# Kernel tuning notes

Hardware: AMD Instinct MI355X
Metric: run time of the kernel (lower is better)

The kernel has to match this reference:

```python
import jax, jax.numpy as jnp
import numpy as np

B, L, D, H = 2, 256, 512, 8
DH = D // H
EPS = 1e-12
NEG = -1000000000000000.0


def setup_inputs() -> dict:
    key = jax.random.key(0)
    ks = jax.random.split(key, 16)
    s = 0.02
    return {
        "inputs": jax.random.normal(ks[0], (B, L, D), jnp.float32),
        "pos_embedding": jax.random.normal(ks[1], (B, L, L, D), jnp.float32),
        "seq_mask": jnp.ones((B, L), jnp.int32),
        "Wq": jax.random.normal(ks[2], (D, D), jnp.float32) * s,
        "bq": jnp.zeros((D,), jnp.float32),
        "Wk": jax.random.normal(ks[3], (D, D), jnp.float32) * s,
        "bk": jnp.zeros((D,), jnp.float32),
        "Wv": jax.random.normal(ks[4], (D, D), jnp.float32) * s,
        "bv": jnp.zeros((D,), jnp.float32),
        "Wr": jax.random.normal(ks[5], (D, D), jnp.float32) * s,
        "br": jnp.zeros((D,), jnp.float32),
        "u": jax.random.normal(ks[6], (H, DH), jnp.float32),
        "v": jax.random.normal(ks[7], (H, DH), jnp.float32),
        "Wf": jax.random.normal(ks[8], (D, D), jnp.float32) * s,
        "bf": jnp.zeros((D,), jnp.float32),
        "gamma": jnp.ones((D,), jnp.float32),
        "beta": jnp.zeros((D,), jnp.float32),
    }


def _layer_norm(x, gamma, beta, eps):
    mu = jnp.mean(x, axis=-1, keepdims=True)
    var = jnp.mean(jnp.square(x - mu), axis=-1, keepdims=True)
    return (x - mu) * jax.lax.rsqrt(var + eps) * gamma + beta


def reference(inputs, pos_embedding, seq_mask, Wq, bq, Wk, bk, Wv, bv, Wr, br,
              u, v, Wf, bf, gamma, beta):
    b, l, d = inputs.shape
    # projections (nn.Linear: x @ W.T + b)
    q = (inputs @ Wq.T + bq).reshape(b, l, H, DH).transpose(0, 2, 1, 3)  # [B,H,L,DH]
    k = (inputs @ Wk.T + bk).reshape(b, l, H, DH).transpose(0, 2, 1, 3)
    vv = (inputs @ Wv.T + bv).reshape(b, l, H, DH).transpose(0, 2, 1, 3)
    rel = (pos_embedding @ Wr.T + br).reshape(b, l, l, H, DH)            # [B,L,L,H,DH]

    # A + C: content-content + content-bias
    A_C = jnp.einsum('bhid,bhjd->bhij', q + u[None, :, None, :], k)
    # B + D: position term against per-(i,j) relative embeddings
    B_D = jnp.einsum('bhid,bijhd->bhij', q + v[None, :, None, :], rel)

    score = (A_C + B_D) / np.sqrt(DH).astype(np.float32)
    invalid = (seq_mask == 0)[:, None, None, :]   # mask keys where seq_mask==0
    score = jnp.where(invalid, NEG, score)
    attn = jax.nn.softmax(score, axis=-1)

    ctx = jnp.einsum('bhij,bhjd->bhid', attn, vv)
    ctx = ctx.transpose(0, 2, 1, 3).reshape(b, l, d)

    # FFN (single dense) + residual + LayerNorm
    h = ctx @ Wf.T + bf
    return _layer_norm(h + inputs, gamma, beta, EPS)
```

## Files before the change

### kernel.cpp

```cpp
#include <hip/hip_runtime.h>
#include <cmath>

typedef __bf16 bf16x8 __attribute__((ext_vector_type(8)));
typedef float f32x4 __attribute__((ext_vector_type(4)));

__device__ __forceinline__ float4 ld4(const float* p) { return *reinterpret_cast<const float4*>(p); }
__device__ __forceinline__ void st4(float* p, float4 v) { *reinterpret_cast<float4*>(p) = v; }
__device__ __forceinline__ void fma4(float4& a, float s, const float4& v) {
    a.x = fmaf(s, v.x, a.x); a.y = fmaf(s, v.y, a.y);
    a.z = fmaf(s, v.z, a.z); a.w = fmaf(s, v.w, a.w);
}
__device__ __forceinline__ float dot4(const float4& a, const float4& b) {
    return a.x*b.x + a.y*b.y + a.z*b.z + a.w*b.w;
}
__device__ __forceinline__ unsigned short f2bf(float f) {
    unsigned int x = __float_as_uint(f);
    unsigned int r = x + 0x7FFFu + ((x >> 16) & 1u);
    return (unsigned short)(r >> 16);
}
__device__ __forceinline__ ushort4 cvt4u(float4 a) {
    ushort4 u;
    u.x = f2bf(a.x); u.y = f2bf(a.y); u.z = f2bf(a.z); u.w = f2bf(a.w);
    return u;
}
__device__ __forceinline__ bf16x8 cvt8(float4 a, float4 b) {
    bf16x8 r;
    r[0] = (__bf16)a.x; r[1] = (__bf16)a.y; r[2] = (__bf16)a.z; r[3] = (__bf16)a.w;
    r[4] = (__bf16)b.x; r[5] = (__bf16)b.y; r[6] = (__bf16)b.z; r[7] = (__bf16)b.w;
    return r;
}

__device__ __forceinline__ void mfma_tile(
        const float* __restrict__ Abase, int ldA,
        const float* __restrict__ Bbase, int ldB,
        int K, int lane, f32x4 acc[4]) {
    int koff = (lane >> 4) * 8;
    int rr = lane & 15;
    const float* ap = Abase + rr * ldA + koff;
    const float* bp = Bbase + rr * ldB + koff;
#pragma unroll 2
    for (int k0 = 0; k0 < K; k0 += 32) {
        float4 a0  = ld4(ap + k0),            a1  = ld4(ap + k0 + 4);
        float4 b00 = ld4(bp + k0),            b01 = ld4(bp + k0 + 4);
        float4 b10 = ld4(bp + 16*ldB + k0),   b11 = ld4(bp + 16*ldB + k0 + 4);
        float4 b20 = ld4(bp + 32*ldB + k0),   b21 = ld4(bp + 32*ldB + k0 + 4);
        float4 b30 = ld4(bp + 48*ldB + k0),   b31 = ld4(bp + 48*ldB + k0 + 4);
        bf16x8 af = cvt8(a0, a1);
        acc[0] = __builtin_amdgcn_mfma_f32_16x16x32_bf16(af, cvt8(b00, b01), acc[0], 0, 0, 0);
        acc[1] = __builtin_amdgcn_mfma_f32_16x16x32_bf16(af, cvt8(b10, b11), acc[1], 0, 0, 0);
        acc[2] = __builtin_amdgcn_mfma_f32_16x16x32_bf16(af, cvt8(b20, b21), acc[2], 0, 0, 0);
        acc[3] = __builtin_amdgcn_mfma_f32_16x16x32_bf16(af, cvt8(b30, b31), acc[3], 0, 0, 0);
    }
}

__global__ __launch_bounds__(256) void k_front(
        const float* __restrict__ x,
        const float* __restrict__ Wq, const float* __restrict__ Wk, const float* __restrict__ Wv,
        const float* __restrict__ bq, const float* __restrict__ bk, const float* __restrict__ bv,
        const float* __restrict__ Wr,
        float* __restrict__ qw, float* __restrict__ kw, float* __restrict__ vw,
        float* __restrict__ wrt) {
    int id = blockIdx.x;
    int t = threadIdx.x;
    if (id < 192) {
        int mat = id >> 6, rem = id & 63;
        int m0 = (rem >> 3) * 64, n0 = (rem & 7) * 64;
        const float* W   = (mat == 0) ? Wq : (mat == 1) ? Wk : Wv;
        const float* bias= (mat == 0) ? bq : (mat == 1) ? bk : bv;
        float* out       = (mat == 0) ? qw : (mat == 1) ? kw : vw;
        int wv = t >> 6, lane = t & 63;
        f32x4 acc[4] = {{0,0,0,0},{0,0,0,0},{0,0,0,0},{0,0,0,0}};
        mfma_tile(x + (m0 + wv * 16) * 512, 512, W + n0 * 512, 512, 512, lane, acc);
        int h = n0 >> 6;
        int col = lane & 15, rbase = (lane >> 4) * 4;
#pragma unroll
        for (int c = 0; c < 4; c++) {
            int d = c * 16 + col;
            float bv_ = bias[n0 + d];
#pragma unroll
            for (int r = 0; r < 4; r++) {
                int m = m0 + wv * 16 + rbase + r;
                int b = m >> 8, i = m & 255;
                out[((b * 8 + h) * 256 + i) * 64 + d] = acc[c][r] + bv_;
            }
        }
    } else {
        __shared__ float tile[64][65];
        int id2 = id - 192;
        int n0 = (id2 >> 3) * 64, k0 = (id2 & 7) * 64;
        int tx = t & 63, ty = t >> 6;
#pragma unroll
        for (int r = 0; r < 16; r++) {
            int row = ty * 16 + r;
            tile[row][tx] = Wr[(n0 + row) * 512 + k0 + tx];
        }
        __syncthreads();
#pragma unroll
        for (int r = 0; r < 16; r++) {
            int row = ty * 16 + r;
            wrt[(k0 + row) * 512 + n0 + tx] = tile[tx][row];
        }
    }
}

__global__ __launch_bounds__(256) void k_mid(
        const float* __restrict__ qw, const float* __restrict__ kw,
        const float* __restrict__ wrt,
        const float* __restrict__ u, const float* __restrict__ vb, const float* __restrict__ br,
        float* __restrict__ w_ws, float* __restrict__ ac_ws) {
    int id = blockIdx.x;
    int t = threadIdx.x, wv = t >> 6, lane = t & 63;
    __shared__ float red[8][64];
    if (id < 512) {
        int h = id >> 6, rem = id & 63;
        int m0 = (rem >> 3) * 64, n0 = (rem & 7) * 64;
        int b = m0 >> 8, i0 = m0 & 255;
        {
            int e = t & 63, grp = t >> 6;
            const float* wr_row = wrt + (size_t)(n0 + e) * 512 + h * 64 + grp * 16;
            const float* vbh = vb + h * 64 + grp * 16;
            float s = 0.f;
#pragma unroll
            for (int d = 0; d < 16; d += 4) s += dot4(ld4(wr_row + d), ld4(vbh + d));
            red[grp][e] = s;
        }
        __syncthreads();
        __shared__ float vwr_l[64];
        if (t < 64) vwr_l[t] = red[0][t] + red[1][t] + red[2][t] + red[3][t];
        f32x4 acc[4] = {{0,0,0,0},{0,0,0,0},{0,0,0,0},{0,0,0,0}};
        mfma_tile(qw + ((b * 8 + h) * 256 + i0 + wv * 16) * 64, 64,
                  wrt + (size_t)n0 * 512 + h * 64, 512, 64, lane, acc);
        __syncthreads();
        int col = lane & 15, rbase = (lane >> 4) * 4;
#pragma unroll
        for (int c = 0; c < 4; c++) {
            float vw_ = vwr_l[c * 16 + col];
            int n = n0 + c * 16 + col;
#pragma unroll
            for (int r = 0; r < 4; r++) {
                int m = m0 + wv * 16 + rbase + r;
                w_ws[((size_t)m * 8 + h) * 512 + n] = acc[c][r] + vw_;
            }
        }
    } else {
        int id2 = id - 512;
        int bh = id2 >> 4, rem2 = id2 & 15;
        int b = bh >> 3, h = bh & 7;
        int i0 = (rem2 >> 2) * 64, j0 = (rem2 & 3) * 64;
        {
            int xx = t & 63, grp = t >> 6;
            const float* qrow = qw + ((b * 8 + h) * 256 + i0 + xx) * 64 + grp * 16;
            const float* brh = br + h * 64 + grp * 16;
            const float* vbh = vb + h * 64 + grp * 16;
            float s = 0.f;
#pragma unroll
            for (int d = 0; d < 16; d += 4) {
                float4 q4 = ld4(qrow + d), b4 = ld4(brh + d), v4 = ld4(vbh + d);
                s += (q4.x + v4.x) * b4.x + (q4.y + v4.y) * b4.y
                   + (q4.z + v4.z) * b4.z + (q4.w + v4.w) * b4.w;
            }
            red[grp][xx] = s;
            const float* krow = kw + ((b * 8 + h) * 256 + j0 + xx) * 64 + grp * 16;
            const float* uh = u + h * 64 + grp * 16;
            s = 0.f;
#pragma unroll
            for (int d = 0; d < 16; d += 4) s += dot4(ld4(krow + d), ld4(uh + d));
            red[4 + grp][xx] = s;
        }
        __syncthreads();
        __shared__ float c_l[64], uk_l[64];
        if (t < 64) c_l[t] = red[0][t] + red[1][t] + red[2][t] + red[3][t];
        else if (t < 128) { int y = t - 64; uk_l[y] = red[4][y] + red[5][y] + red[6][y] + red[7][y]; }
        f32x4 acc[4] = {{0,0,0,0},{0,0,0,0},{0,0,0,0},{0,0,0,0}};
        mfma_tile(qw + ((b * 8 + h) * 256 + i0 + wv * 16) * 64, 64,
                  kw + ((b * 8 + h) * 256 + j0) * 64, 64, 64, lane, acc);
        __syncthreads();
        int col = lane & 15, rbase = (lane >> 4) * 4;
#pragma unroll
        for (int c = 0; c < 4; c++) {
            int j = j0 + c * 16 + col;
            float ukv = uk_l[c * 16 + col];
#pragma unroll
            for (int r = 0; r < 4; r++) {
                int ii = wv * 16 + rbase + r;
                ac_ws[((b * 256 + i0 + ii) * 8 + h) * 256 + j] = acc[c][r] + ukv + c_l[ii];
            }
        }
    }
}

__global__ __launch_bounds__(512, 4) void k_attn(
        const float* __restrict__ pos, const float* __restrict__ w_ws,
        const float* __restrict__ ac_ws, const float* __restrict__ vw,
        const int* __restrict__ seq_mask, float* __restrict__ ctx) {
    int bi = blockIdx.x;
    int b = bi >> 8, i = bi & 255;
    int t = threadIdx.x;
    int wv = t >> 6, lane = t & 63;
    __shared__ unsigned short wl[8 * 512];
    __shared__ float sc[8][256];
    __shared__ unsigned short stage[8][4096];

    {
        int h = t >> 6;
        int e0 = (t & 63) * 8;
        const float* src = w_ws + ((size_t)bi * 8 + h) * 512 + e0;
        float4 a = ld4(src);
        float4 c = ld4(src + 4);
        *reinterpret_cast<ushort4*>(&wl[h * 512 + e0])     = cvt4u(a);
        *reinterpret_cast<ushort4*>(&wl[h * 512 + e0 + 4]) = cvt4u(c);
    }
    __syncthreads();

    const float* pb = pos + (size_t)bi * (256 * 512);
    int jbase = wv * 32;
    unsigned short* sb = &stage[wv][0];
    int arow = lane & 15;
    int koff = (lane >> 4) * 8;

#pragma unroll
    for (int jt = 0; jt < 2; jt++) {
        f32x4 acc = {0, 0, 0, 0};
#pragma unroll
        for (int eh = 0; eh < 2; eh++) {
            const float* src = pb + (size_t)(jbase + jt * 16) * 512 + eh * 256 + lane * 4;
            float4 tmp[16];
#pragma unroll
            for (int s = 0; s < 16; s++) tmp[s] = ld4(src + s * 512);
#pragma unroll
            for (int s = 0; s < 16; s++) {
                *reinterpret_cast<ushort4*>(&sb[s * 256 + lane * 4]) = cvt4u(tmp[s]);
            }
#pragma unroll
            for (int es = 0; es < 8; es++) {
                bf16x8 af = *reinterpret_cast<const bf16x8*>(&sb[arow * 256 + es * 32 + koff]);
                bf16x8 bf = *reinterpret_cast<const bf16x8*>(&wl[(lane & 7) * 512 + (eh * 8 + es) * 32 + koff]);
                acc = __builtin_amdgcn_mfma_f32_16x16x32_bf16(af, bf, acc, 0, 0, 0);
            }
        }
        int h = lane & 15;
        int rbase = (lane >> 4) * 4;
        if (h < 8) {
#pragma unroll
            for (int r = 0; r < 4; r++) sc[h][jbase + jt * 16 + rbase + r] = acc[r];
        }
    }
    __syncthreads();

    {
        int h = wv;
        const float* acrow = ac_ws + ((b * 256 + i) * 8 + h) * 256;
        float vals[4];
        float mx = -INFINITY;
#pragma unroll
        for (int r = 0; r < 4; r++) {
            int j = lane + r * 64;
            float s = (sc[h][j] + acrow[j]) * 0.125f;
            if (seq_mask[b * 256 + j] == 0) s = -1e15f;
            vals[r] = s;
            mx = fmaxf(mx, s);
        }
#pragma unroll
        for (int m = 32; m >= 1; m >>= 1) mx = fmaxf(mx, __shfl_xor(mx, m, 64));
        float sum = 0.f;
#pragma unroll
        for (int r = 0; r < 4; r++) { vals[r] = __expf(vals[r] - mx); sum += vals[r]; }
#pragma unroll
        for (int m = 32; m >= 1; m >>= 1) sum += __shfl_xor(sum, m, 64);
        float inv = 1.0f / sum;
#pragma unroll
        for (int r = 0; r < 4; r++) sc[h][lane + r * 64] = vals[r] * inv;
    }

    float4* part = reinterpret_cast<float4*>(&stage[0][0]);
    {
        int h = wv;
        int d4 = (lane & 15) * 4;
        int js = lane >> 4;
        const float* vbase = vw + (size_t)(b * 8 + h) * 256 * 64 + d4;
        float4 acc = {0, 0, 0, 0};
#pragma unroll 2
        for (int r = 0; r < 64; r += 4) {
            int j = js * 64 + r;
            float p0 = sc[h][j + 0], p1 = sc[h][j + 1];
            float p2 = sc[h][j + 2], p3 = sc[h][j + 3];
            float4 v0 = ld4(vbase + (size_t)(j + 0) * 64);
            float4 v1 = ld4(vbase + (size_t)(j + 1) * 64);
            float4 v2 = ld4(vbase + (size_t)(j + 2) * 64);
            float4 v3 = ld4(vbase + (size_t)(j + 3) * 64);
            fma4(acc, p0, v0); fma4(acc, p1, v1);
            fma4(acc, p2, v2); fma4(acc, p3, v3);
        }
        part[(h * 4 + js) * 16 + (lane & 15)] = acc;
    }
    {
        int h = wv;
        if ((lane >> 4) == 0) {
            int l = lane & 15;
            float4 a0 = part[(h * 4 + 0) * 16 + l], a1 = part[(h * 4 + 1) * 16 + l];
            float4 a2 = part[(h * 4 + 2) * 16 + l], a3 = part[(h * 4 + 3) * 16 + l];
            float4 o;
            o.x = a0.x + a1.x + a2.x + a3.x;
            o.y = a0.y + a1.y + a2.y + a3.y;
            o.z = a0.z + a1.z + a2.z + a3.z;
            o.w = a0.w + a1.w + a2.w + a3.w;
            st4(ctx + (size_t)(b * 256 + i) * 512 + h * 64 + l * 4, o);
        }
    }
}

__global__ __launch_bounds__(256) void k_ffn(
        const float* __restrict__ A, const float* __restrict__ Wf,
        const float* __restrict__ bias, const float* __restrict__ resid,
        float* __restrict__ outp) {
    int m0 = blockIdx.x * 64, n0 = blockIdx.y * 64;
    int t = threadIdx.x, wv = t >> 6, lane = t & 63;
    f32x4 acc[4] = {{0,0,0,0},{0,0,0,0},{0,0,0,0},{0,0,0,0}};
    mfma_tile(A + (m0 + wv * 16) * 512, 512, Wf + n0 * 512, 512, 512, lane, acc);
    int col = lane & 15, rbase = (lane >> 4) * 4;
#pragma unroll
    for (int c = 0; c < 4; c++) {
        int n = n0 + c * 16 + col;
        float bv_ = bias[n];
#pragma unroll
        for (int r = 0; r < 4; r++) {
            int m = m0 + wv * 16 + rbase + r;
            outp[m * 512 + n] = acc[c][r] + bv_ + resid[m * 512 + n];
        }
    }
}

__global__ __launch_bounds__(256) void k_ln(
        const float* __restrict__ tmp, const float* __restrict__ gamma,
        const float* __restrict__ beta, float* __restrict__ out) {
    int m = blockIdx.x, t = threadIdx.x;
    int wv = t >> 6, lane = t & 63;
    float2 xv = *reinterpret_cast<const float2*>(&tmp[m * 512 + t * 2]);
    __shared__ float red[4];
    float s = xv.x + xv.y;
#pragma unroll
    for (int k = 32; k >= 1; k >>= 1) s += __shfl_xor(s, k, 64);
    if (lane == 0) red[wv] = s;
    __syncthreads();
    float mu = (red[0] + red[1] + red[2] + red[3]) * (1.0f / 512.0f);
    __syncthreads();
    float dx = xv.x - mu, dy = xv.y - mu;
    float vs = dx * dx + dy * dy;
#pragma unroll
    for (int k = 32; k >= 1; k >>= 1) vs += __shfl_xor(vs, k, 64);
    if (lane == 0) red[wv] = vs;
    __syncthreads();
    float var = (red[0] + red[1] + red[2] + red[3]) * (1.0f / 512.0f);
    float rstd = rsqrtf(var + 1e-12f);
    float2 g = *reinterpret_cast<const float2*>(&gamma[t * 2]);
    float2 be = *reinterpret_cast<const float2*>(&beta[t * 2]);
    float2 o;
    o.x = dx * rstd * g.x + be.x;
    o.y = dy * rstd * g.y + be.y;
    *reinterpret_cast<float2*>(&out[m * 512 + t * 2]) = o;
}

extern "C" void kernel_launch(void* const* d_in, const int* in_sizes, int n_in,
                              void* d_out, int out_size, void* d_ws, size_t ws_size,
                              hipStream_t stream) {
    const float* x     = (const float*)d_in[0];
    const float* pos   = (const float*)d_in[1];
    const int*   smask = (const int*)d_in[2];
    const float* Wq = (const float*)d_in[3];
    const float* bq = (const float*)d_in[4];
    const float* Wk = (const float*)d_in[5];
    const float* bk = (const float*)d_in[6];
    const float* Wv = (const float*)d_in[7];
    const float* bv = (const float*)d_in[8];
    const float* Wr = (const float*)d_in[9];
    const float* br = (const float*)d_in[10];
    const float* u  = (const float*)d_in[11];
    const float* vb = (const float*)d_in[12];
    const float* Wf = (const float*)d_in[13];
    const float* bf = (const float*)d_in[14];
    const float* gamma = (const float*)d_in[15];
    const float* beta  = (const float*)d_in[16];
    float* out = (float*)d_out;

    float* ws = (float*)d_ws;
    float* q_ws   = ws;
    float* k_ws   = q_ws  + 262144;
    float* v_ws   = k_ws  + 262144;
    float* w_ws   = v_ws  + 262144;
    float* ac_ws  = w_ws  + 2097152;
    float* ctx_ws = ac_ws + 1048576;
    float* tmp_ws = ctx_ws + 262144;
    float* wrt_ws = tmp_ws + 262144;

    k_front<<<dim3(256), 256, 0, stream>>>(x, Wq, Wk, Wv, bq, bk, bv, Wr,
                                           q_ws, k_ws, v_ws, wrt_ws);
    k_mid<<<dim3(768), 256, 0, stream>>>(q_ws, k_ws, wrt_ws, u, vb, br, w_ws, ac_ws);
    k_attn<<<dim3(512), 512, 0, stream>>>(pos, w_ws, ac_ws, v_ws, smask, ctx_ws);
    k_ffn<<<dim3(8, 8), 256, 0, stream>>>(ctx_ws, Wf, bf, x, tmp_ws);
    k_ln<<<dim3(512), 256, 0, stream>>>(tmp_ws, gamma, beta, out);
}
```

Measured before the change: 110.7 us.

## Fuse FFN with LayerNorm, drop Wr transpose, swizzle attention LDS staging

Removes the separate Wr transpose pass: k_mid reads Wr directly with strided scalar loads, and the (q+v)·br bias term moves into the Q projection epilogue. The u·k and v·Wr terms are folded into the MFMA A operand by adding the bias vectors before conversion. In k_attn the staging buffer is halved, an XOR swizzle is applied to LDS addresses to reduce bank conflicts, and the occupancy hint goes from 4 to 6. The FFN and LayerNorm kernels are fused into one 32-block kernel that computes LN statistics with a single-pass sum/sumsq. Risks are low parallelism in the fused output kernel, uncoalesced Wr reads, and sumsq variance cancellation.

```diff
diff --git a/kernel.cpp b/kernel.cpp
--- a/kernel.cpp
+++ b/kernel.cpp
@@ -5,14 +5,12 @@
 typedef float f32x4 __attribute__((ext_vector_type(4)));
 
 __device__ __forceinline__ float4 ld4(const float* p) { return *reinterpret_cast<const float4*>(p); }
+__device__ __forceinline__ float2 ld2(const float* p) { return *reinterpret_cast<const float2*>(p); }
 __device__ __forceinline__ void st4(float* p, float4 v) { *reinterpret_cast<float4*>(p) = v; }
 __device__ __forceinline__ void fma4(float4& a, float s, const float4& v) {
     a.x = fmaf(s, v.x, a.x); a.y = fmaf(s, v.y, a.y);
     a.z = fmaf(s, v.z, a.z); a.w = fmaf(s, v.w, a.w);
 }
-__device__ __forceinline__ float dot4(const float4& a, const float4& b) {
-    return a.x*b.x + a.y*b.y + a.z*b.z + a.w*b.w;
-}
 __device__ __forceinline__ unsigned short f2bf(float f) {
     unsigned int x = __float_as_uint(f);
     unsigned int r = x + 0x7FFFu + ((x >> 16) & 1u);
@@ -22,6 +20,9 @@
     ushort4 u;
     u.x = f2bf(a.x); u.y = f2bf(a.y); u.z = f2bf(a.z); u.w = f2bf(a.w);
     return u;
+}
+__device__ __forceinline__ ushort2 cvt2u(float2 a) {
+    ushort2 u; u.x = f2bf(a.x); u.y = f2bf(a.y); return u;
 }
 __device__ __forceinline__ bf16x8 cvt8(float4 a, float4 b) {
     bf16x8 r;
@@ -57,139 +58,139 @@
         const float* __restrict__ x,
         const float* __restrict__ Wq, const float* __restrict__ Wk, const float* __restrict__ Wv,
         const float* __restrict__ bq, const float* __restrict__ bk, const float* __restrict__ bv,
-        const float* __restrict__ Wr,
+        const float* __restrict__ vbv, const float* __restrict__ br,
         float* __restrict__ qw, float* __restrict__ kw, float* __restrict__ vw,
-        float* __restrict__ wrt) {
+        float* __restrict__ c_ws) {
     int id = blockIdx.x;
     int t = threadIdx.x;
-    if (id < 192) {
-        int mat = id >> 6, rem = id & 63;
-        int m0 = (rem >> 3) * 64, n0 = (rem & 7) * 64;
-        const float* W   = (mat == 0) ? Wq : (mat == 1) ? Wk : Wv;
-        const float* bias= (mat == 0) ? bq : (mat == 1) ? bk : bv;
-        float* out       = (mat == 0) ? qw : (mat == 1) ? kw : vw;
-        int wv = t >> 6, lane = t & 63;
-        f32x4 acc[4] = {{0,0,0,0},{0,0,0,0},{0,0,0,0},{0,0,0,0}};
-        mfma_tile(x + (m0 + wv * 16) * 512, 512, W + n0 * 512, 512, 512, lane, acc);
-        int h = n0 >> 6;
-        int col = lane & 15, rbase = (lane >> 4) * 4;
-#pragma unroll
-        for (int c = 0; c < 4; c++) {
-            int d = c * 16 + col;
-            float bv_ = bias[n0 + d];
+    int mat = id >> 6, rem = id & 63;
+    int m0 = (rem >> 3) * 64, n0 = (rem & 7) * 64;
+    const float* W   = (mat == 0) ? Wq : (mat == 1) ? Wk : Wv;
+    const float* bias= (mat == 0) ? bq : (mat == 1) ? bk : bv;
+    float* out       = (mat == 0) ? qw : (mat == 1) ? kw : vw;
+    int wv = t >> 6, lane = t & 63;
+    f32x4 acc[4] = {{0,0,0,0},{0,0,0,0},{0,0,0,0},{0,0,0,0}};
+    mfma_tile(x + (m0 + wv * 16) * 512, 512, W + n0 * 512, 512, 512, lane, acc);
+    int h = n0 >> 6;
+    int col = lane & 15, rbase = (lane >> 4) * 4;
+    float cpart[4] = {0, 0, 0, 0};
+#pragma unroll
+    for (int c = 0; c < 4; c++) {
+        int d = c * 16 + col;
+        float bv_ = bias[n0 + d];
+        float vbd = vbv[n0 + d];
+        float brd = br[n0 + d];
+#pragma unroll
+        for (int r = 0; r < 4; r++) {
+            int m = m0 + wv * 16 + rbase + r;
+            int b = m >> 8, i = m & 255;
+            float q = acc[c][r] + bv_;
+            out[((b * 8 + h) * 256 + i) * 64 + d] = q;
+            cpart[r] += (q + vbd) * brd;
+        }
+    }
+    if (mat == 0) {
+#pragma unroll
+        for (int msk = 1; msk < 16; msk <<= 1) {
+#pragma unroll
+            for (int r = 0; r < 4; r++) cpart[r] += __shfl_xor(cpart[r], msk, 64);
+        }
+        if (col == 0) {
 #pragma unroll
             for (int r = 0; r < 4; r++) {
                 int m = m0 + wv * 16 + rbase + r;
                 int b = m >> 8, i = m & 255;
-                out[((b * 8 + h) * 256 + i) * 64 + d] = acc[c][r] + bv_;
-            }
-        }
-    } else {
-        __shared__ float tile[64][65];
-        int id2 = id - 192;
-        int n0 = (id2 >> 3) * 64, k0 = (id2 & 7) * 64;
-        int tx = t & 63, ty = t >> 6;
-#pragma unroll
-        for (int r = 0; r < 16; r++) {
-            int row = ty * 16 + r;
-            tile[row][tx] = Wr[(n0 + row) * 512 + k0 + tx];
-        }
-        __syncthreads();
-#pragma unroll
-        for (int r = 0; r < 16; r++) {
-            int row = ty * 16 + r;
-            wrt[(k0 + row) * 512 + n0 + tx] = tile[tx][row];
+                c_ws[(b * 8 + h) * 256 + i] = cpart[r];
+            }
         }
     }
 }
 
 __global__ __launch_bounds__(256) void k_mid(
         const float* __restrict__ qw, const float* __restrict__ kw,
-        const float* __restrict__ wrt,
-        const float* __restrict__ u, const float* __restrict__ vb, const float* __restrict__ br,
+        const float* __restrict__ Wr,
+        const float* __restrict__ u, const float* __restrict__ vbv,
+        const float* __restrict__ c_ws,
         float* __restrict__ w_ws, float* __restrict__ ac_ws) {
     int id = blockIdx.x;
     int t = threadIdx.x, wv = t >> 6, lane = t & 63;
-    __shared__ float red[8][64];
-    if (id < 512) {
-        int h = id >> 6, rem = id & 63;
-        int m0 = (rem >> 3) * 64, n0 = (rem & 7) * 64;
+    int rr = lane & 15, koff = (lane >> 4) * 8;
+    int col = lane & 15, rbase = (lane >> 4) * 4;
+    if (id < 256) {
+        int h = id >> 5, rem = id & 31;
+        int it = rem >> 2, et2 = rem & 3;
+        int m0 = it * 64, E0 = et2 * 128;
         int b = m0 >> 8, i0 = m0 & 255;
-        {
-            int e = t & 63, grp = t >> 6;
-            const float* wr_row = wrt + (size_t)(n0 + e) * 512 + h * 64 + grp * 16;
-            const float* vbh = vb + h * 64 + grp * 16;
-            float s = 0.f;
-#pragma unroll
-            for (int d = 0; d < 16; d += 4) s += dot4(ld4(wr_row + d), ld4(vbh + d));
-            red[grp][e] = s;
-        }
-        __syncthreads();
-        __shared__ float vwr_l[64];
-        if (t < 64) vwr_l[t] = red[0][t] + red[1][t] + red[2][t] + red[3][t];
-        f32x4 acc[4] = {{0,0,0,0},{0,0,0,0},{0,0,0,0},{0,0,0,0}};
-        mfma_tile(qw + ((b * 8 + h) * 256 + i0 + wv * 16) * 64, 64,
-                  wrt + (size_t)n0 * 512 + h * 64, 512, 64, lane, acc);
-        __syncthreads();
-        int col = lane & 15, rbase = (lane >> 4) * 4;
-#pragma unroll
-        for (int c = 0; c < 4; c++) {
-            float vw_ = vwr_l[c * 16 + col];
-            int n = n0 + c * 16 + col;
+        const float* ap = qw + (size_t)((b * 8 + h) * 256 + i0 + wv * 16 + rr) * 64;
+        const float* vb_p = vbv + h * 64;
+        f32x4 acc[8];
+#pragma unroll
+        for (int nt = 0; nt < 8; nt++) acc[nt] = (f32x4){0, 0, 0, 0};
+#pragma unroll
+        for (int k0 = 0; k0 < 64; k0 += 32) {
+            float4 a0 = ld4(ap + k0 + koff), a1 = ld4(ap + k0 + koff + 4);
+            float4 v0 = ld4(vb_p + k0 + koff), v1 = ld4(vb_p + k0 + koff + 4);
+            a0.x += v0.x; a0.y += v0.y; a0.z += v0.z; a0.w += v0.w;
+            a1.x += v1.x; a1.y += v1.y; a1.z += v1.z; a1.w += v1.w;
+            bf16x8 af = cvt8(a0, a1);
+            const float* wrb = Wr + (size_t)(h * 64 + k0 + koff) * 512 + E0 + rr;
+#pragma unroll
+            for (int nt = 0; nt < 8; nt++) {
+                bf16x8 bf_;
+#pragma unroll
+                for (int kk = 0; kk < 8; kk++)
+                    bf_[kk] = (__bf16)wrb[(size_t)kk * 512 + nt * 16];
+                acc[nt] = __builtin_amdgcn_mfma_f32_16x16x32_bf16(af, bf_, acc[nt], 0, 0, 0);
+            }
+        }
+#pragma unroll
+        for (int nt = 0; nt < 8; nt++) {
+            int e = E0 + nt * 16 + col;
 #pragma unroll
             for (int r = 0; r < 4; r++) {
                 int m = m0 + wv * 16 + rbase + r;
-                w_ws[((size_t)m * 8 + h) * 512 + n] = acc[c][r] + vw_;
+                w_ws[((size_t)m * 8 + h) * 512 + e] = acc[nt][r];
             }
         }
     } else {
-        int id2 = id - 512;
-        int bh = id2 >> 4, rem2 = id2 & 15;
+        int id2 = id - 256;
+        int bh = id2 >> 3, rem = id2 & 7;
         int b = bh >> 3, h = bh & 7;
-        int i0 = (rem2 >> 2) * 64, j0 = (rem2 & 3) * 64;
-        {
-            int xx = t & 63, grp = t >> 6;
-            const float* qrow = qw + ((b * 8 + h) * 256 + i0 + xx) * 64 + grp * 16;
-            const float* brh = br + h * 64 + grp * 16;
-            const float* vbh = vb + h * 64 + grp * 16;
-            float s = 0.f;
-#pragma unroll
-            for (int d = 0; d < 16; d += 4) {
-                float4 q4 = ld4(qrow + d), b4 = ld4(brh + d), v4 = ld4(vbh + d);
-                s += (q4.x + v4.x) * b4.x + (q4.y + v4.y) * b4.y
-                   + (q4.z + v4.z) * b4.z + (q4.w + v4.w) * b4.w;
-            }
-            red[grp][xx] = s;
-            const float* krow = kw + ((b * 8 + h) * 256 + j0 + xx) * 64 + grp * 16;
-            const float* uh = u + h * 64 + grp * 16;
-            s = 0.f;
-#pragma unroll
-            for (int d = 0; d < 16; d += 4) s += dot4(ld4(krow + d), ld4(uh + d));
-            red[4 + grp][xx] = s;
-        }
-        __syncthreads();
-        __shared__ float c_l[64], uk_l[64];
-        if (t < 64) c_l[t] = red[0][t] + red[1][t] + red[2][t] + red[3][t];
-        else if (t < 128) { int y = t - 64; uk_l[y] = red[4][y] + red[5][y] + red[6][y] + red[7][y]; }
-        f32x4 acc[4] = {{0,0,0,0},{0,0,0,0},{0,0,0,0},{0,0,0,0}};
-        mfma_tile(qw + ((b * 8 + h) * 256 + i0 + wv * 16) * 64, 64,
-                  kw + ((b * 8 + h) * 256 + j0) * 64, 64, 64, lane, acc);
-        __syncthreads();
-        int col = lane & 15, rbase = (lane >> 4) * 4;
-#pragma unroll
-        for (int c = 0; c < 4; c++) {
-            int j = j0 + c * 16 + col;
-            float ukv = uk_l[c * 16 + col];
-#pragma unroll
-            for (int r = 0; r < 4; r++) {
-                int ii = wv * 16 + rbase + r;
-                ac_ws[((b * 256 + i0 + ii) * 8 + h) * 256 + j] = acc[c][r] + ukv + c_l[ii];
-            }
-        }
-    }
-}
-
-__global__ __launch_bounds__(512, 4) void k_attn(
+        int i0 = (rem >> 1) * 64, J0 = (rem & 1) * 128;
+        const float* ap = qw + (size_t)((b * 8 + h) * 256 + i0 + wv * 16 + rr) * 64;
+        const float* up = u + h * 64;
+        const float* kbase = kw + (size_t)((b * 8 + h) * 256 + J0) * 64;
+        f32x4 acc[8];
+#pragma unroll
+        for (int nt = 0; nt < 8; nt++) acc[nt] = (f32x4){0, 0, 0, 0};
+#pragma unroll
+        for (int k0 = 0; k0 < 64; k0 += 32) {
+            float4 a0 = ld4(ap + k0 + koff), a1 = ld4(ap + k0 + koff + 4);
+            float4 u0 = ld4(up + k0 + koff), u1 = ld4(up + k0 + koff + 4);
+            a0.x += u0.x; a0.y += u0.y; a0.z += u0.z; a0.w += u0.w;
+            a1.x += u1.x; a1.y += u1.y; a1.z += u1.z; a1.w += u1.w;
+            bf16x8 af = cvt8(a0, a1);
+#pragma unroll
+            for (int nt = 0; nt < 8; nt++) {
+                const float* kp = kbase + (size_t)(nt * 16 + rr) * 64 + k0 + koff;
+                bf16x8 bf_ = cvt8(ld4(kp), ld4(kp + 4));
+                acc[nt] = __builtin_amdgcn_mfma_f32_16x16x32_bf16(af, bf_, acc[nt], 0, 0, 0);
+            }
+        }
+#pragma unroll
+        for (int r = 0; r < 4; r++) {
+            int i = i0 + wv * 16 + rbase + r;
+            float ci = c_ws[(b * 8 + h) * 256 + i];
+#pragma unroll
+            for (int nt = 0; nt < 8; nt++) {
+                int j = J0 + nt * 16 + col;
+                ac_ws[((size_t)(b * 256 + i) * 8 + h) * 256 + j] = acc[nt][r] + ci;
+            }
+        }
+    }
+}
+
+__global__ __launch_bounds__(512, 6) void k_attn(
         const float* __restrict__ pos, const float* __restrict__ w_ws,
         const float* __restrict__ ac_ws, const float* __restrict__ vw,
         const int* __restrict__ seq_mask, float* __restrict__ ctx) {
@@ -199,22 +200,22 @@
     int wv = t >> 6, lane = t & 63;
     __shared__ unsigned short wl[8 * 512];
     __shared__ float sc[8][256];
-    __shared__ unsigned short stage[8][4096];
+    __shared__ unsigned short stage[8][2048];
 
     {
         int h = t >> 6;
         int e0 = (t & 63) * 8;
         const float* src = w_ws + ((size_t)bi * 8 + h) * 512 + e0;
-        float4 a = ld4(src);
-        float4 c = ld4(src + 4);
-        *reinterpret_cast<ushort4*>(&wl[h * 512 + e0])     = cvt4u(a);
-        *reinterpret_cast<ushort4*>(&wl[h * 512 + e0 + 4]) = cvt4u(c);
+        float4 a = ld4(src), c = ld4(src + 4);
+        int byte = ((h * 512 + e0) * 2) ^ ((h & 7) << 4);
+        *reinterpret_cast<ushort4*>(reinterpret_cast<char*>(wl) + byte)     = cvt4u(a);
+        *reinterpret_cast<ushort4*>(reinterpret_cast<char*>(wl) + byte + 8) = cvt4u(c);
     }
     __syncthreads();
 
     const float* pb = pos + (size_t)bi * (256 * 512);
     int jbase = wv * 32;
-    unsigned short* sb = &stage[wv][0];
+    char* sb = reinterpret_cast<char*>(&stage[wv][0]);
     int arow = lane & 15;
     int koff = (lane >> 4) * 8;
 
@@ -222,20 +223,25 @@
     for (int jt = 0; jt < 2; jt++) {
         f32x4 acc = {0, 0, 0, 0};
 #pragma unroll
-        for (int eh = 0; eh < 2; eh++) {
-            const float* src = pb + (size_t)(jbase + jt * 16) * 512 + eh * 256 + lane * 4;
-            float4 tmp[16];
-#pragma unroll
-            for (int s = 0; s < 16; s++) tmp[s] = ld4(src + s * 512);
+        for (int eh = 0; eh < 4; eh++) {
+            const float* src = pb + (size_t)(jbase + jt * 16) * 512 + eh * 128 + lane * 2;
+            float2 tmp[16];
+#pragma unroll
+            for (int s = 0; s < 16; s++) tmp[s] = ld2(src + (size_t)s * 512);
 #pragma unroll
             for (int s = 0; s < 16; s++) {
-                *reinterpret_cast<ushort4*>(&sb[s * 256 + lane * 4]) = cvt4u(tmp[s]);
-            }
-#pragma unroll
-            for (int es = 0; es < 8; es++) {
-                bf16x8 af = *reinterpret_cast<const bf16x8*>(&sb[arow * 256 + es * 32 + koff]);
-                bf16x8 bf = *reinterpret_cast<const bf16x8*>(&wl[(lane & 7) * 512 + (eh * 8 + es) * 32 + koff]);
-                acc = __builtin_amdgcn_mfma_f32_16x16x32_bf16(af, bf, acc, 0, 0, 0);
+                int byte = (256 * s + 4 * lane) ^ ((s & 7) << 4);
+                *reinterpret_cast<ushort2*>(sb + byte) = cvt2u(tmp[s]);
+            }
+#pragma unroll
+            for (int es = 0; es < 4; es++) {
+                int ab = (256 * arow + 64 * es + 2 * koff) ^ ((arow & 7) << 4);
+                bf16x8 af = *reinterpret_cast<const bf16x8*>(sb + ab);
+                int estep = eh * 4 + es;
+                int wb = (((lane & 7) * 512 + estep * 32 + koff) * 2) ^ ((lane & 7) << 4);
+                bf16x8 bf_ = *reinterpret_cast<const bf16x8*>(
+                    reinterpret_cast<const char*>(wl) + wb);
+                acc = __builtin_amdgcn_mfma_f32_16x16x32_bf16(af, bf_, acc, 0, 0, 0);
             }
         }
         int h = lane & 15;
@@ -309,55 +315,84 @@
     }
 }
 
-__global__ __launch_bounds__(256) void k_ffn(
+__global__ __launch_bounds__(256) void k_out(
         const float* __restrict__ A, const float* __restrict__ Wf,
-        const float* __restrict__ bias, const float* __restrict__ resid,
+        const float* __restrict__ bf, const float* __restrict__ resid,
+        const float* __restrict__ gamma, const float* __restrict__ beta,
         float* __restrict__ outp) {
-    int m0 = blockIdx.x * 64, n0 = blockIdx.y * 64;
+    int m0 = blockIdx.x * 16;
     int t = threadIdx.x, wv = t >> 6, lane = t & 63;
-    f32x4 acc[4] = {{0,0,0,0},{0,0,0,0},{0,0,0,0},{0,0,0,0}};
-    mfma_tile(A + (m0 + wv * 16) * 512, 512, Wf + n0 * 512, 512, 512, lane, acc);
+    int rr = lane & 15, koff = (lane >> 4) * 8;
     int col = lane & 15, rbase = (lane >> 4) * 4;
-#pragma unroll
-    for (int c = 0; c < 4; c++) {
-        int n = n0 + c * 16 + col;
-        float bv_ = bias[n];
-#pragma unroll
-        for (int r = 0; r < 4; r++) {
-            int m = m0 + wv * 16 + rbase + r;
-            outp[m * 512 + n] = acc[c][r] + bv_ + resid[m * 512 + n];
-        }
-    }
-}
-
-__global__ __launch_bounds__(256) void k_ln(
-        const float* __restrict__ tmp, const float* __restrict__ gamma,
-        const float* __restrict__ beta, float* __restrict__ out) {
-    int m = blockIdx.x, t = threadIdx.x;
-    int wv = t >> 6, lane = t & 63;
-    float2 xv = *reinterpret_cast<const float2*>(&tmp[m * 512 + t * 2]);
-    __shared__ float red[4];
-    float s = xv.x + xv.y;
-#pragma unroll
-    for (int k = 32; k >= 1; k >>= 1) s += __shfl_xor(s, k, 64);
-    if (lane == 0) red[wv] = s;
+    const float* ap = A + (size_t)(m0 + rr) * 512 + koff;
+    f32x4 acc[8];
+#pragma unroll
+    for (int nt = 0; nt < 8; nt++) acc[nt] = (f32x4){0, 0, 0, 0};
+#pragma unroll 2
+    for (int k0 = 0; k0 < 512; k0 += 32) {
+        float4 a0 = ld4(ap + k0), a1 = ld4(ap + k0 + 4);
+        bf16x8 af = cvt8(a0, a1);
+#pragma unroll
+        for (int nt = 0; nt < 8; nt++) {
+            int n = wv * 128 + nt * 16 + rr;
+            float4 b0 = ld4(&Wf[(size_t)n * 512 + k0 + koff]);
+            float4 b1 = ld4(&Wf[(size_t)n * 512 + k0 + koff + 4]);
+            acc[nt] = __builtin_amdgcn_mfma_f32_16x16x32_bf16(af, cvt8(b0, b1), acc[nt], 0, 0, 0);
+        }
+    }
+    float vals[8][4];
+    float psum[4] = {0, 0, 0, 0}, psq[4] = {0, 0, 0, 0};
+#pragma unroll
+    for (int nt = 0; nt < 8; nt++) {
+        int n = wv * 128 + nt * 16 + col;
+        float bfn = bf[n];
+#pragma unroll
+        for (int r = 0; r < 4; r++) {
+            int m = m0 + rbase + r;
+            float v = acc[nt][r] + bfn + resid[(size_t)m * 512 + n];
+            vals[nt][r] = v;
+            psum[r] += v;
+            psq[r] += v * v;
+        }
+    }
+#pragma unroll
+    for (int msk = 1; msk < 16; msk <<= 1) {
+#pragma unroll
+        for (int r = 0; r < 4; r++) {
+            psum[r] += __shfl_xor(psum[r], msk, 64);
+            psq[r]  += __shfl_xor(psq[r],  msk, 64);
+        }
+    }
+    __shared__ float redS[16][4], redQ[16][4];
+    if ((lane & 15) == 0) {
+#pragma unroll
+        for (int r = 0; r < 4; r++) {
+            redS[rbase + r][wv] = psum[r];
+            redQ[rbase + r][wv] = psq[r];
+        }
+    }
     __syncthreads();
-    float mu = (red[0] + red[1] + red[2] + red[3]) * (1.0f / 512.0f);
-    __syncthreads();
-    float dx = xv.x - mu, dy = xv.y - mu;
-    float vs = dx * dx + dy * dy;
-#pragma unroll
-    for (int k = 32; k >= 1; k >>= 1) vs += __shfl_xor(vs, k, 64);
-    if (lane == 0) red[wv] = vs;
-    __syncthreads();
-    float var = (red[0] + red[1] + red[2] + red[3]) * (1.0f / 512.0f);
-    float rstd = rsqrtf(var + 1e-12f);
-    float2 g = *reinterpret_cast<const float2*>(&gamma[t * 2]);
-    float2 be = *reinterpret_cast<const float2*>(&beta[t * 2]);
-    float2 o;
-    o.x = dx * rstd * g.x + be.x;
-    o.y = dy * rstd * g.y + be.y;
-    *reinterpret_cast<float2*>(&out[m * 512 + t * 2]) = o;
+    float mu[4], rstd[4];
+#pragma unroll
+    for (int r = 0; r < 4; r++) {
+        int row = rbase + r;
+        float s = redS[row][0] + redS[row][1] + redS[row][2] + redS[row][3];
+        float q = redQ[row][0] + redQ[row][1] + redQ[row][2] + redQ[row][3];
+        float m_ = s * (1.0f / 512.0f);
+        float var = q * (1.0f / 512.0f) - m_ * m_;
+        mu[r] = m_;
+        rstd[r] = rsqrtf(var + 1e-12f);
+    }
+#pragma unroll
+    for (int nt = 0; nt < 8; nt++) {
+        int n = wv * 128 + nt * 16 + col;
+        float g = gamma[n], be = beta[n];
+#pragma unroll
+        for (int r = 0; r < 4; r++) {
+            int m = m0 + rbase + r;
+            outp[(size_t)m * 512 + n] = (vals[nt][r] - mu[r]) * rstd[r] * g + be;
+        }
+    }
 }
 
 extern "C" void kernel_launch(void* const* d_in, const int* in_sizes, int n_in,
@@ -386,16 +421,14 @@
     float* q_ws   = ws;
     float* k_ws   = q_ws  + 262144;
     float* v_ws   = k_ws  + 262144;
-    float* w_ws   = v_ws  + 262144;
+    float* c_ws   = v_ws  + 262144;
+    float* w_ws   = c_ws  + 4096;
     float* ac_ws  = w_ws  + 2097152;
     float* ctx_ws = ac_ws + 1048576;
-    float* tmp_ws = ctx_ws + 262144;
-    float* wrt_ws = tmp_ws + 262144;
-
-    k_front<<<dim3(256), 256, 0, stream>>>(x, Wq, Wk, Wv, bq, bk, bv, Wr,
-                                           q_ws, k_ws, v_ws, wrt_ws);
-    k_mid<<<dim3(768), 256, 0, stream>>>(q_ws, k_ws, wrt_ws, u, vb, br, w_ws, ac_ws);
+
+    k_front<<<dim3(192), 256, 0, stream>>>(x, Wq, Wk, Wv, bq, bk, bv, vb, br,
+                                           q_ws, k_ws, v_ws, c_ws);
+    k_mid<<<dim3(384), 256, 0, stream>>>(q_ws, k_ws, Wr, u, vb, c_ws, w_ws, ac_ws);
     k_attn<<<dim3(512), 512, 0, stream>>>(pos, w_ws, ac_ws, v_ws, smask, ctx_ws);
-    k_ffn<<<dim3(8, 8), 256, 0, stream>>>(ctx_ws, Wf, bf, x, tmp_ws);
-    k_ln<<<dim3(512), 256, 0, stream>>>(tmp_ws, gamma, beta, out);
-}
+    k_out<<<dim3(32), 256, 0, stream>>>(ctx_ws, Wf, bf, x, gamma, beta, out);
+}
```

Result: slower. 140.4 us (+26.9%).
